# Optimization experiments

Measured on AMD Instinct MI355X. Metric: run time of the kernel, lower is better.

The kernel has to match this reference:

```python
import jax, jax.numpy as jnp
import numpy as np

B, H, W, C, HEADS = 4, 64, 64, 512, 8
HD = C // HEADS
L = H * W
BIAS_LEVEL = 0.1
LN_EPS = 1e-5


def _ln(x, g, b):
    mu = jnp.mean(x, axis=-1, keepdims=True)
    var = jnp.var(x, axis=-1, keepdims=True)
    return (x - mu) * jax.lax.rsqrt(var + LN_EPS) * g + b


def setup_inputs() -> dict:
    key = jax.random.key(0)
    ks = jax.random.split(key, 16)
    s = 0.02
    return {
        "x": jax.random.normal(ks[0], (B, L, C), jnp.float32),
        "rpe": jax.random.normal(ks[1], (H, HEADS, W, W), jnp.float32),
        "qkv_w": jax.random.normal(ks[2], (3 * C, C), jnp.float32) * s,
        "proj_w": jax.random.normal(ks[3], (C, C), jnp.float32) * s,
        "proj_b": jnp.zeros((C,), jnp.float32),
        "norm1_w": jnp.ones((C,), jnp.float32),
        "norm1_b": jnp.zeros((C,), jnp.float32),
        "norm2_w": jnp.ones((C,), jnp.float32),
        "norm2_b": jnp.zeros((C,), jnp.float32),
        "fc1_w": jax.random.normal(ks[4], (4 * C, C), jnp.float32) * s,
        "fc1_b": jnp.zeros((4 * C,), jnp.float32),
        "fc2_w": jax.random.normal(ks[5], (C, 4 * C), jnp.float32) * s,
        "fc2_b": jnp.zeros((C,), jnp.float32),
    }


def reference(x, rpe, qkv_w, proj_w, proj_b, norm1_w, norm1_b, norm2_w, norm2_b,
              fc1_w, fc1_b, fc2_w, fc2_b):
    # --- qkv projection ---
    img = _ln(x, norm1_w, norm1_b)
    qkv = (img @ qkv_w.T).reshape(B, L, 3, C)
    q, k, v = qkv[:, :, 0], qkv[:, :, 1], qkv[:, :, 2]

    # idx=0 horizontal windows: each row of the HxW grid is a window of len W.
    def to_win(t):  # (B, L, C) -> (B*H, heads, W, hd)
        return t.reshape(B * H, W, HEADS, HD).transpose(0, 2, 1, 3)

    qw, kw, vw = to_win(q), to_win(k), to_win(v)

    # attention scores + relative position bias (RPE tiled over batch)
    attn = jnp.einsum('whqd,whkd->whqk', qw, kw)
    attn = attn + BIAS_LEVEL * jnp.tile(rpe, (B, 1, 1, 1))

    # magnitude gate M per window
    M = jnp.mean(jnp.abs(attn), axis=(1, 2, 3), keepdims=True)  # (B*H,1,1,1)
    M = M / jnp.max(M)
    M = jnp.maximum(M, 0.5)

    # cosine-based score transform: 1 - cos(pi/2 * l2normalize(attn))
    nrm = jnp.maximum(jnp.linalg.norm(attn, axis=-1, keepdims=True), 1e-12)
    attn = 1.0 - jnp.cos((attn / nrm) * (jnp.pi / 2.0))
    attn = attn * M

    o = jnp.einsum('whqk,whkd->whqd', attn, vw)  # (B*H, heads, W, hd)
    o = o.transpose(0, 2, 1, 3).reshape(B, L, C)

    # residual gating by (1 - M)
    res = (x.reshape(B * H, 1, W, C) * (1.0 - M)).reshape(B, L, C)
    attened = o + res

    attened = attened @ proj_w.T + proj_b
    x1 = x + attened

    h = _ln(x1, norm2_w, norm2_b)
    h = jax.nn.gelu(h @ fc1_w.T + fc1_b, approximate=False)
    h = h @ fc2_w.T + fc2_b
    return x1 + h
```

## Files before the change

kernel.cpp:

```cpp
#include <hip/hip_runtime.h>
#include <hip/hip_bf16.h>
#include <math.h>

typedef unsigned short u16;
typedef __bf16 bf16x8 __attribute__((ext_vector_type(8)));
typedef float f32x4 __attribute__((ext_vector_type(4)));
typedef unsigned short u16x8 __attribute__((ext_vector_type(8)));

typedef const __attribute__((address_space(1))) void* gas_ptr;
typedef __attribute__((address_space(3))) void* las_ptr;

__device__ __forceinline__ float bf2f(u16 u) {
    union { unsigned int i; float f; } x;
    x.i = ((unsigned int)u) << 16;
    return x.f;
}
__device__ __forceinline__ u16 f2bf(float f) {
    __hip_bfloat16 h = __float2bfloat16(f);
    return __builtin_bit_cast(u16, h);
}
__device__ __forceinline__ __bf16 f2bfr(float f) {
    __hip_bfloat16 h = __float2bfloat16(f);
    return __builtin_bit_cast(__bf16, h);
}
__device__ __forceinline__ void load_lds16(const void* g, void* l) {
    __builtin_amdgcn_global_load_lds((gas_ptr)g, (las_ptr)l, 16, 0, 0);
}

__global__ __launch_bounds__(256) void cvt_all_k(const float* __restrict__ qkv_w,
                                                 const float* __restrict__ proj_w,
                                                 const float* __restrict__ fc1w,
                                                 const float* __restrict__ fc2w,
                                                 u16* __restrict__ wqkv,
                                                 u16* __restrict__ wproj,
                                                 u16* __restrict__ wfc1,
                                                 u16* __restrict__ wfc2) {
    const int b = blockIdx.x;
    const float* src; u16* dst; int off;
    if (b < 768)       { src = qkv_w;  dst = wqkv;  off = b; }
    else if (b < 1024) { src = proj_w; dst = wproj; off = b - 768; }
    else if (b < 2048) { src = fc1w;   dst = wfc1;  off = b - 1024; }
    else               { src = fc2w;   dst = wfc2;  off = b - 2048; }
    const int i = off * 256 + threadIdx.x;
    const float4 v = ((const float4*)src)[i];
    ushort4 o;
    o.x = f2bf(v.x); o.y = f2bf(v.y); o.z = f2bf(v.z); o.w = f2bf(v.w);
    ((ushort4*)dst)[i] = o;
}

template<bool BF16IN>
__global__ __launch_bounds__(256) void ln_k(const void* __restrict__ inp,
                                            const float* __restrict__ gw,
                                            const float* __restrict__ gb,
                                            u16* __restrict__ outp) {
    const int row = blockIdx.x, t = threadIdx.x;
    float v0, v1;
    if (BF16IN) {
        const u16* rp = (const u16*)inp + (size_t)row * 512;
        v0 = bf2f(rp[2 * t]); v1 = bf2f(rp[2 * t + 1]);
    } else {
        const float2 v = ((const float2*)((const float*)inp + (size_t)row * 512))[t];
        v0 = v.x; v1 = v.y;
    }
    float s = v0 + v1, q = v0 * v0 + v1 * v1;
    #pragma unroll
    for (int o = 1; o < 64; o <<= 1) {
        s += __shfl_xor(s, o);
        q += __shfl_xor(q, o);
    }
    __shared__ float rs[4], rq[4];
    const int w = t >> 6;
    if ((t & 63) == 0) { rs[w] = s; rq[w] = q; }
    __syncthreads();
    s = rs[0] + rs[1] + rs[2] + rs[3];
    q = rq[0] + rq[1] + rq[2] + rq[3];
    const float mean = s * (1.0f / 512.0f);
    const float var = q * (1.0f / 512.0f) - mean * mean;
    const float rstd = rsqrtf(var + 1e-5f);
    u16* op = outp + (size_t)row * 512;
    op[2 * t]     = f2bf((v0 - mean) * rstd * gw[2 * t]     + gb[2 * t]);
    op[2 * t + 1] = f2bf((v1 - mean) * rstd * gw[2 * t + 1] + gb[2 * t + 1]);
}

template<int EPI, bool AFUSE>
__global__ __launch_bounds__(256) void gemm_bt(const u16* __restrict__ A,
                                               const u16* __restrict__ W,
                                               const float* __restrict__ bias,
                                               const float* __restrict__ res_f,
                                               const u16* __restrict__ res_bf,
                                               void* __restrict__ outp,
                                               int M, int N, int K,
                                               const float* __restrict__ aM,
                                               const u16* __restrict__ aO,
                                               const float* __restrict__ aX) {
    __shared__ __bf16 As[2][128 * 32];
    __shared__ __bf16 Bs[2][128 * 32];
    const int t = threadIdx.x;
    const int l = t & 63;
    const int w = t >> 6;
    const int wm = w & 1, wn = w >> 1;
    const int bm = blockIdx.x * 128, bn = blockIdx.y * 128;

    f32x4 acc[4][4] = {};

    auto stage = [&](int buf, int kt) {
        #pragma unroll
        for (int p = 0; p < 2; ++p) {
            const int slot = p * 256 + t;
            const int row = slot >> 2;
            const int gl = (slot & 3) ^ ((row >> 1) & 3);
            if (AFUSE) {
                const int grow = bm + row;
                const size_t gidx = (size_t)grow * K + kt + gl * 8;
                const float Mw = aM[grow >> 6];
                const float rf = 1.0f - Mw;
                const u16x8 ov = *(const u16x8*)(aO + gidx);
                const float4 x0 = *(const float4*)(aX + gidx);
                const float4 x1 = *(const float4*)(aX + gidx + 4);
                bf16x8 val;
                val[0] = f2bfr(Mw * bf2f(ov[0]) + rf * x0.x);
                val[1] = f2bfr(Mw * bf2f(ov[1]) + rf * x0.y);
                val[2] = f2bfr(Mw * bf2f(ov[2]) + rf * x0.z);
                val[3] = f2bfr(Mw * bf2f(ov[3]) + rf * x0.w);
                val[4] = f2bfr(Mw * bf2f(ov[4]) + rf * x1.x);
                val[5] = f2bfr(Mw * bf2f(ov[5]) + rf * x1.y);
                val[6] = f2bfr(Mw * bf2f(ov[6]) + rf * x1.z);
                val[7] = f2bfr(Mw * bf2f(ov[7]) + rf * x1.w);
                *(bf16x8*)&As[buf][slot * 8] = val;
            } else {
                load_lds16(A + (size_t)(bm + row) * K + kt + gl * 8,
                           &As[buf][p * 2048 + w * 512]);
            }
            load_lds16(W + (size_t)(bn + row) * K + kt + gl * 8,
                       &Bs[buf][p * 2048 + w * 512]);
        }
    };

    const int nk = K >> 5;
    stage(0, 0);
    __syncthreads();
    for (int s = 0; s < nk; ++s) {
        if (s + 1 < nk) stage((s + 1) & 1, (s + 1) << 5);
        const int buf = s & 1;
        const int r = l & 15, g = l >> 4;
        bf16x8 af[4], bfr[4];
        #pragma unroll
        for (int i = 0; i < 4; ++i) {
            const int ra = wm * 64 + i * 16 + r;
            af[i] = *(const bf16x8*)&As[buf][ra * 32 + ((g ^ ((ra >> 1) & 3)) << 3)];
            const int rb = wn * 64 + i * 16 + r;
            bfr[i] = *(const bf16x8*)&Bs[buf][rb * 32 + ((g ^ ((rb >> 1) & 3)) << 3)];
        }
        #pragma unroll
        for (int i = 0; i < 4; ++i)
            #pragma unroll
            for (int j = 0; j < 4; ++j)
                acc[i][j] = __builtin_amdgcn_mfma_f32_16x16x32_bf16(af[i], bfr[j], acc[i][j], 0, 0, 0);
        __syncthreads();
    }

    #pragma unroll
    for (int i = 0; i < 4; ++i) {
        #pragma unroll
        for (int j = 0; j < 4; ++j) {
            #pragma unroll
            for (int rr = 0; rr < 4; ++rr) {
                const int m = bm + wm * 64 + i * 16 + ((l >> 4) << 2) + rr;
                const int n = bn + wn * 64 + j * 16 + (l & 15);
                float v = acc[i][j][rr];
                const size_t idx = (size_t)m * N + n;
                if (EPI == 0) {
                    ((u16*)outp)[idx] = f2bf(v);
                } else if (EPI == 1) {
                    ((u16*)outp)[idx] = f2bf(v + bias[n] + res_f[idx]);
                } else if (EPI == 2) {
                    v += bias[n];
                    v = 0.5f * v * (1.0f + erff(v * 0.70710678118654752f));
                    ((u16*)outp)[idx] = f2bf(v);
                } else {
                    ((float*)outp)[idx] = v + bias[n] + bf2f(res_bf[idx]);
                }
            }
        }
    }
}

__global__ __launch_bounds__(256) void attn_k(const u16* __restrict__ qkv,
                                              const float* __restrict__ rpe,
                                              float* __restrict__ Mpart,
                                              u16* __restrict__ Obuf) {
    const int blk = blockIdx.x;
    const int wh = blk >> 3, head = blk & 7;
    const int himg = wh & 63;
    const int t = threadIdx.x, l = t & 63, w = t >> 6;
    __shared__ __bf16 Qs[4096];
    __shared__ __bf16 Ks[4096];
    __shared__ __bf16 Vt[4096];
    __shared__ __bf16 Ps[4096];
    __shared__ float red[4];

    #pragma unroll
    for (int p = 0; p < 2; ++p) {
        const int sb = (p * 256 + t) << 4;
        const int row = sb >> 7;
        const int gl = ((sb >> 4) & 7) ^ (row & 7);
        const size_t gsrc = (size_t)(wh * 64 + row) * 1536 + head * 64 + gl * 8;
        const int lbase = p * 2048 + w * 512;
        load_lds16(qkv + gsrc, &Qs[lbase]);
        load_lds16(qkv + gsrc + 512, &Ks[lbase]);
    }
    {
        const int k = t >> 2, dc = (t & 3) * 16;
        const u16* vr = qkv + (size_t)(wh * 64 + k) * 1536 + 1024 + head * 64 + dc;
        u16x8 v0 = *(const u16x8*)vr;
        u16x8 v1 = *(const u16x8*)(vr + 8);
        const int g = k >> 3, klo = k & 7;
        #pragma unroll
        for (int i = 0; i < 8; ++i) {
            const int d0 = dc + i, d1 = dc + 8 + i;
            Vt[d0 * 64 + ((g ^ (d0 & 7)) << 3) + klo] = __builtin_bit_cast(__bf16, (u16)v0[i]);
            Vt[d1 * 64 + ((g ^ (d1 & 7)) << 3) + klo] = __builtin_bit_cast(__bf16, (u16)v1[i]);
        }
    }
    __syncthreads();

    const int r = l & 15, g4 = l >> 4;
    f32x4 acc[4] = {};
    #pragma unroll
    for (int h = 0; h < 2; ++h) {
        const int rowq = w * 16 + r;
        bf16x8 aq = *(const bf16x8*)&Qs[rowq * 64 + (((h * 4 + g4) ^ (rowq & 7)) << 3)];
        #pragma unroll
        for (int j = 0; j < 4; ++j) {
            const int rowk = j * 16 + r;
            bf16x8 bk = *(const bf16x8*)&Ks[rowk * 64 + (((h * 4 + g4) ^ (rowk & 7)) << 3)];
            acc[j] = __builtin_amdgcn_mfma_f32_16x16x32_bf16(aq, bk, acc[j], 0, 0, 0);
        }
    }

    float v[4][4];
    float asum = 0.f;
    float ss[4] = {0.f, 0.f, 0.f, 0.f};
    const size_t rpe_base = (size_t)(himg * 8 + head) * 4096 + (size_t)(w * 16 + g4 * 4) * 64 + r;
    #pragma unroll
    for (int j = 0; j < 4; ++j) {
        #pragma unroll
        for (int rr = 0; rr < 4; ++rr) {
            const float val = acc[j][rr] + 0.1f * rpe[rpe_base + rr * 64 + j * 16];
            v[j][rr] = val;
            asum += fabsf(val);
            ss[rr] += val * val;
        }
    }
    #pragma unroll
    for (int m = 1; m < 16; m <<= 1) {
        #pragma unroll
        for (int rr = 0; rr < 4; ++rr) ss[rr] += __shfl_xor(ss[rr], m);
    }
    float srev[4];
    #pragma unroll
    for (int rr = 0; rr < 4; ++rr)
        srev[rr] = 0.25f / fmaxf(sqrtf(ss[rr]), 1e-12f);

    #pragma unroll
    for (int j = 0; j < 4; ++j) {
        #pragma unroll
        for (int rr = 0; rr < 4; ++rr) {
            const float pv = 1.0f - __builtin_amdgcn_cosf(v[j][rr] * srev[rr]);
            const int rl = g4 * 4 + rr;
            const int c = j * 16 + r;
            Ps[w * 1024 + rl * 64 + (((c >> 3) ^ (rl & 7)) << 3) + (c & 7)] = f2bfr(pv);
        }
    }

    f32x4 oacc[4] = {};
    #pragma unroll
    for (int ks = 0; ks < 2; ++ks) {
        const int ga = ks * 4 + g4;
        bf16x8 pa = *(const bf16x8*)&Ps[w * 1024 + r * 64 + ((ga ^ (r & 7)) << 3)];
        #pragma unroll
        for (int j = 0; j < 4; ++j) {
            const int d = j * 16 + r;
            bf16x8 vb = *(const bf16x8*)&Vt[d * 64 + ((ga ^ (d & 7)) << 3)];
            oacc[j] = __builtin_amdgcn_mfma_f32_16x16x32_bf16(pa, vb, oacc[j], 0, 0, 0);
        }
    }

    #pragma unroll
    for (int j = 0; j < 4; ++j) {
        #pragma unroll
        for (int rr = 0; rr < 4; ++rr) {
            const int token = wh * 64 + w * 16 + g4 * 4 + rr;
            Obuf[(size_t)token * 512 + head * 64 + j * 16 + r] = f2bf(oacc[j][rr]);
        }
    }

    #pragma unroll
    for (int o = 1; o < 64; o <<= 1) asum += __shfl_xor(asum, o);
    if (l == 0) red[w] = asum;
    __syncthreads();
    if (t == 0) Mpart[blk] = red[0] + red[1] + red[2] + red[3];
}

__global__ __launch_bounds__(256) void mfinal_k(const float* __restrict__ Mpart,
                                                float* __restrict__ M) {
    const int t = threadIdx.x;
    float m = 0.f;
    #pragma unroll
    for (int h = 0; h < 8; ++h) m += Mpart[t * 8 + h];
    m *= (1.0f / 32768.0f);
    float mx = m;
    #pragma unroll
    for (int o = 1; o < 64; o <<= 1) mx = fmaxf(mx, __shfl_xor(mx, o));
    __shared__ float red[4];
    if ((t & 63) == 0) red[t >> 6] = mx;
    __syncthreads();
    mx = fmaxf(fmaxf(red[0], red[1]), fmaxf(red[2], red[3]));
    M[t] = fmaxf(m / mx, 0.5f);
}

extern "C" void kernel_launch(void* const* d_in, const int* in_sizes, int n_in,
                              void* d_out, int out_size, void* d_ws, size_t ws_size,
                              hipStream_t stream) {
    (void)in_sizes; (void)n_in; (void)out_size; (void)ws_size;
    const float* x      = (const float*)d_in[0];
    const float* rpe    = (const float*)d_in[1];
    const float* qkv_w  = (const float*)d_in[2];
    const float* proj_w = (const float*)d_in[3];
    const float* proj_b = (const float*)d_in[4];
    const float* n1w    = (const float*)d_in[5];
    const float* n1b    = (const float*)d_in[6];
    const float* n2w    = (const float*)d_in[7];
    const float* n2b    = (const float*)d_in[8];
    const float* fc1w   = (const float*)d_in[9];
    const float* fc1b   = (const float*)d_in[10];
    const float* fc2w   = (const float*)d_in[11];
    const float* fc2b   = (const float*)d_in[12];
    float* out = (float*)d_out;

    char* ws = (char*)d_ws;
    float* Mpart = (float*)ws;
    float* Mbuf  = (float*)(ws + 8192);
    u16* wqkv  = (u16*)(ws + 16384);
    u16* wproj = (u16*)(ws + 16384 + 1572864);
    u16* wfc1  = (u16*)(ws + 16384 + 2097152);
    u16* wfc2  = (u16*)(ws + 16384 + 4194304);
    u16* bufA  = (u16*)(ws + 6307840);
    u16* bufB  = (u16*)(ws + 23085056);
    char* R    = ws + 39862272;
    u16*   qkvb = (u16*)R;
    u16*   Obuf = (u16*)(R + 50331648);
    u16*   gbuf = (u16*)R;

    cvt_all_k<<<3072, 256, 0, stream>>>(qkv_w, proj_w, fc1w, fc2w,
                                        wqkv, wproj, wfc1, wfc2);
    ln_k<false><<<16384, 256, 0, stream>>>(x, n1w, n1b, bufA);
    gemm_bt<0, false><<<dim3(128, 12), 256, 0, stream>>>(
        bufA, wqkv, nullptr, nullptr, nullptr, qkvb, 16384, 1536, 512,
        nullptr, nullptr, nullptr);
    attn_k<<<2048, 256, 0, stream>>>(qkvb, rpe, Mpart, Obuf);
    mfinal_k<<<1, 256, 0, stream>>>(Mpart, Mbuf);
    gemm_bt<1, true><<<dim3(128, 4), 256, 0, stream>>>(
        nullptr, wproj, proj_b, x, nullptr, bufA, 16384, 512, 512,
        Mbuf, Obuf, x);
    ln_k<true><<<16384, 256, 0, stream>>>(bufA, n2w, n2b, bufB);
    gemm_bt<2, false><<<dim3(128, 16), 256, 0, stream>>>(
        bufB, wfc1, fc1b, nullptr, nullptr, gbuf, 16384, 2048, 512,
        nullptr, nullptr, nullptr);
    gemm_bt<3, false><<<dim3(128, 4), 256, 0, stream>>>(
        gbuf, wfc2, fc2b, nullptr, bufA, out, 16384, 512, 2048,
        nullptr, nullptr, nullptr);
}
```

Baseline: 207.4 us.

## Double GEMM K-tile to 64 with 8-way swizzle and polynomial erf GELU

The GEMM K step grows from 32 to 64. LDS tiles double in size and use a new XOR swizzle over 8 chunks, with precomputed per-thread base pointers for staging, which halves the number of loop iterations and barriers. Separately, the exact erff in the fc1 GELU epilogue is replaced with the Abramowitz-Stegun polynomial approximation using __expf. The trade-offs are higher LDS use per block (64KB), which may lower occupancy, and a small accuracy loss in GELU.

```diff
diff --git a/kernel.cpp b/kernel.cpp
--- a/kernel.cpp
+++ b/kernel.cpp
@@ -25,6 +25,17 @@
 }
 __device__ __forceinline__ void load_lds16(const void* g, void* l) {
     __builtin_amdgcn_global_load_lds((gas_ptr)g, (las_ptr)l, 16, 0, 0);
+}
+__device__ __forceinline__ float gelu_f(float v) {
+    const float a = fabsf(v) * 0.70710678118654752f;
+    const float tt = 1.0f / fmaf(0.3275911f, a, 1.0f);
+    float poly = fmaf(tt, 1.061405429f, -1.453152027f);
+    poly = fmaf(tt, poly, 1.421413741f);
+    poly = fmaf(tt, poly, -0.284496736f);
+    poly = fmaf(tt, poly, 0.254829592f);
+    const float erfa = 1.0f - poly * tt * __expf(-a * a);
+    const float erfv = copysignf(erfa, v);
+    return 0.5f * v * (1.0f + erfv);
 }
 
 __global__ __launch_bounds__(256) void cvt_all_k(const float* __restrict__ qkv_w,
@@ -93,26 +104,30 @@
                                                const float* __restrict__ aM,
                                                const u16* __restrict__ aO,
                                                const float* __restrict__ aX) {
-    __shared__ __bf16 As[2][128 * 32];
-    __shared__ __bf16 Bs[2][128 * 32];
+    __shared__ __bf16 As[2][128 * 64];
+    __shared__ __bf16 Bs[2][128 * 64];
     const int t = threadIdx.x;
     const int l = t & 63;
     const int w = t >> 6;
     const int wm = w & 1, wn = w >> 1;
     const int bm = blockIdx.x * 128, bn = blockIdx.y * 128;
+    const int r = l & 15, g4 = l >> 4;
 
     f32x4 acc[4][4] = {};
 
+    const int rowS = t >> 3;
+    const int cS = (t & 7) ^ (rowS & 7);
+    const size_t rstep = (size_t)32 * K;
+    const u16* wBase = W + (size_t)(bn + rowS) * K + cS * 8;
+    const u16* aBase = AFUSE ? nullptr : (A + (size_t)(bm + rowS) * K + cS * 8);
+    const size_t afBase = (size_t)(bm + rowS) * K + cS * 8;
+
     auto stage = [&](int buf, int kt) {
         #pragma unroll
-        for (int p = 0; p < 2; ++p) {
-            const int slot = p * 256 + t;
-            const int row = slot >> 2;
-            const int gl = (slot & 3) ^ ((row >> 1) & 3);
+        for (int j = 0; j < 4; ++j) {
             if (AFUSE) {
-                const int grow = bm + row;
-                const size_t gidx = (size_t)grow * K + kt + gl * 8;
-                const float Mw = aM[grow >> 6];
+                const size_t gidx = afBase + j * rstep + kt;
+                const float Mw = aM[(bm + rowS + j * 32) >> 6];
                 const float rf = 1.0f - Mw;
                 const u16x8 ov = *(const u16x8*)(aO + gidx);
                 const float4 x0 = *(const float4*)(aX + gidx);
@@ -126,36 +141,39 @@
                 val[5] = f2bfr(Mw * bf2f(ov[5]) + rf * x1.y);
                 val[6] = f2bfr(Mw * bf2f(ov[6]) + rf * x1.z);
                 val[7] = f2bfr(Mw * bf2f(ov[7]) + rf * x1.w);
-                *(bf16x8*)&As[buf][slot * 8] = val;
+                *(bf16x8*)&As[buf][(j * 256 + t) * 8] = val;
             } else {
-                load_lds16(A + (size_t)(bm + row) * K + kt + gl * 8,
-                           &As[buf][p * 2048 + w * 512]);
+                load_lds16(aBase + j * rstep + kt, &As[buf][(j * 256 + t) * 8]);
             }
-            load_lds16(W + (size_t)(bn + row) * K + kt + gl * 8,
-                       &Bs[buf][p * 2048 + w * 512]);
+            load_lds16(wBase + j * rstep + kt, &Bs[buf][(j * 256 + t) * 8]);
         }
     };
 
-    const int nk = K >> 5;
+    const int nk = K >> 6;
     stage(0, 0);
     __syncthreads();
     for (int s = 0; s < nk; ++s) {
-        if (s + 1 < nk) stage((s + 1) & 1, (s + 1) << 5);
+        if (s + 1 < nk) stage((s + 1) & 1, (s + 1) << 6);
         const int buf = s & 1;
-        const int r = l & 15, g = l >> 4;
-        bf16x8 af[4], bfr[4];
+        bf16x8 af[4][2], bfr[4][2];
         #pragma unroll
         for (int i = 0; i < 4; ++i) {
             const int ra = wm * 64 + i * 16 + r;
-            af[i] = *(const bf16x8*)&As[buf][ra * 32 + ((g ^ ((ra >> 1) & 3)) << 3)];
             const int rb = wn * 64 + i * 16 + r;
-            bfr[i] = *(const bf16x8*)&Bs[buf][rb * 32 + ((g ^ ((rb >> 1) & 3)) << 3)];
+            #pragma unroll
+            for (int h = 0; h < 2; ++h) {
+                af[i][h]  = *(const bf16x8*)&As[buf][ra * 64 + (((h * 4 + g4) ^ (ra & 7)) << 3)];
+                bfr[i][h] = *(const bf16x8*)&Bs[buf][rb * 64 + (((h * 4 + g4) ^ (rb & 7)) << 3)];
+            }
         }
         #pragma unroll
         for (int i = 0; i < 4; ++i)
             #pragma unroll
             for (int j = 0; j < 4; ++j)
-                acc[i][j] = __builtin_amdgcn_mfma_f32_16x16x32_bf16(af[i], bfr[j], acc[i][j], 0, 0, 0);
+                #pragma unroll
+                for (int h = 0; h < 2; ++h)
+                    acc[i][j] = __builtin_amdgcn_mfma_f32_16x16x32_bf16(
+                        af[i][h], bfr[j][h], acc[i][j], 0, 0, 0);
         __syncthreads();
     }
 
@@ -165,8 +183,8 @@
         for (int j = 0; j < 4; ++j) {
             #pragma unroll
             for (int rr = 0; rr < 4; ++rr) {
-                const int m = bm + wm * 64 + i * 16 + ((l >> 4) << 2) + rr;
-                const int n = bn + wn * 64 + j * 16 + (l & 15);
+                const int m = bm + wm * 64 + i * 16 + g4 * 4 + rr;
+                const int n = bn + wn * 64 + j * 16 + r;
                 float v = acc[i][j][rr];
                 const size_t idx = (size_t)m * N + n;
                 if (EPI == 0) {
@@ -174,9 +192,7 @@
                 } else if (EPI == 1) {
                     ((u16*)outp)[idx] = f2bf(v + bias[n] + res_f[idx]);
                 } else if (EPI == 2) {
-                    v += bias[n];
-                    v = 0.5f * v * (1.0f + erff(v * 0.70710678118654752f));
-                    ((u16*)outp)[idx] = f2bf(v);
+                    ((u16*)outp)[idx] = f2bf(gelu_f(v + bias[n]));
                 } else {
                     ((float*)outp)[idx] = v + bias[n] + bf2f(res_bf[idx]);
                 }
```

Measured after the change: 198.3 us. 1.05x faster.
